# Kernel optimization log

Measured on AMD Instinct MI355X. Metric: run time of the kernel, lower is better.

## Reference

```python
import jax, jax.numpy as jnp
import numpy as np

HEADS = 16
D_K = 64  # hidden_units // heads


def setup_inputs() -> dict:
    key = jax.random.key(0)
    ks = jax.random.split(key, 9)
    B, S, D, H = 4, 2048, 1024, 1024  # batch, seq, in_shape, hidden_units
    inputs = jax.random.normal(ks[0], (B, S, D), dtype=jnp.float32)
    # xavier_normal for weights, default bias init ~ small uniform (use zeros for simplicity of baseline? keep uniform like torch)
    def xavier(k, fan_in, fan_out):
        std = jnp.sqrt(2.0 / (fan_in + fan_out))
        return jax.random.normal(k, (fan_out, fan_in), dtype=jnp.float32) * std
    Wq = xavier(ks[1], D, H)
    Wk = xavier(ks[2], D, H)
    Wv = xavier(ks[3], D, H)
    Wo = xavier(ks[4], H, H)
    bound = 1.0 / jnp.sqrt(D)
    bq = jax.random.uniform(ks[5], (H,), minval=-bound, maxval=bound, dtype=jnp.float32)
    bk = jax.random.uniform(ks[6], (H,), minval=-bound, maxval=bound, dtype=jnp.float32)
    bv = jax.random.uniform(ks[7], (H,), minval=-bound, maxval=bound, dtype=jnp.float32)
    bo = jax.random.uniform(ks[8], (H,), minval=-1.0 / jnp.sqrt(H), maxval=1.0 / jnp.sqrt(H), dtype=jnp.float32)
    return {"inputs": inputs, "Wq": Wq, "bq": bq, "Wk": Wk, "bk": bk,
            "Wv": Wv, "bv": bv, "Wo": Wo, "bo": bo}


def reference(inputs, Wq, bq, Wk, bk, Wv, bv, Wo, bo):
    B, S, _ = inputs.shape
    # QKV projections -> (B, S, heads, d_k)
    def proj(W, b):
        return (inputs @ W.T + b).reshape(B, S, HEADS, D_K)
    q = proj(Wq, bq)
    k = proj(Wk, bk)
    v = proj(Wv, bv)
    scale = 1.0 / jnp.sqrt(jnp.float32(D_K))
    # scores: (B, heads, S, S)
    scores = jnp.einsum('bqhd,bkhd->bhqk', q, k) * scale
    attn = jax.nn.softmax(scores, axis=-1)
    # (B, heads, S, d_k) -> (B, S, heads*d_k)
    ctx = jnp.einsum('bhqk,bkhd->bqhd', attn, v).reshape(B, S, HEADS * D_K)
    out = ctx @ Wo.T + bo
    return out
```

## Files before the change

kernel.cpp:

```cpp
#include <hip/hip_runtime.h>
#include <stdint.h>


using bf16x8 = __attribute__((ext_vector_type(8))) short;
using f32x4  = __attribute__((ext_vector_type(4))) float;
using u32x4  = __attribute__((ext_vector_type(4))) unsigned;

#define QSCALE 0.18033688f

__device__ __forceinline__ unsigned short f2bf(float f) {
    unsigned u = __builtin_bit_cast(unsigned, f);
    u += 0x7fffu + ((u >> 16) & 1u);
    return (unsigned short)(u >> 16);
}

__device__ __forceinline__ unsigned pack2bf(float f0, float f1) {
    unsigned u0 = __builtin_bit_cast(unsigned, f0) + 0x8000u;
    unsigned u1 = __builtin_bit_cast(unsigned, f1) + 0x8000u;
    return __builtin_amdgcn_perm(u1, u0, 0x07060302);
}

__device__ __forceinline__ void gld16(const void* g, void* l) {
    void* gnc = (void*)g;
    __builtin_amdgcn_global_load_lds((__attribute__((address_space(1))) void*)gnc,
                                     (__attribute__((address_space(3))) void*)l,
                                     16, 0, 0);
}

__device__ __forceinline__ int swz(int R, int g) {
    return R * 64 + ((g ^ (R & 7)) << 3);
}

__global__ void castall(const float* __restrict__ X, const float* __restrict__ Wq,
                        const float* __restrict__ Wk, const float* __restrict__ Wv,
                        const float* __restrict__ Wo, unsigned short* __restrict__ Xb,
                        unsigned short* __restrict__ Wqkvb, unsigned short* __restrict__ Wob) {
    const int bx = blockIdx.x;
    const float* src; unsigned short* dst; int idx;
    if (bx < 8192) { src = X; dst = Xb; idx = bx * 256 + threadIdx.x; }
    else {
        const int r = bx - 8192, w = r >> 10;
        idx = (r & 1023) * 256 + threadIdx.x;
        src = (w == 0) ? Wq : (w == 1) ? Wk : (w == 2) ? Wv : Wo;
        dst = (w == 3) ? Wob : Wqkvb + (size_t)w * 1048576;
    }
    float4 v = ((const float4*)src)[idx];
    ((uint2*)dst)[idx] = make_uint2(pack2bf(v.x, v.y), pack2bf(v.z, v.w));
}

__global__ __launch_bounds__(512, 2) void gemm_qkv(const unsigned short* __restrict__ A,
                                                   const unsigned short* __restrict__ Wqkv,
                                                   const float* __restrict__ bq,
                                                   const float* __restrict__ bk,
                                                   const float* __restrict__ bv,
                                                   unsigned short* __restrict__ Qb,
                                                   unsigned short* __restrict__ Kb,
                                                   unsigned short* __restrict__ Vt) {
    __shared__ alignas(16) unsigned short smem[65536];

    const int tid  = threadIdx.x;
    const int lane = tid & 63;
    const int w    = tid >> 6;
    const int quad = lane >> 4;
    const int l15  = lane & 15;
    const int lr   = lane >> 3;
    const int lcs  = (((lane & 7) ^ lr) << 3);
    const int wm   = w >> 2;
    const int wn   = w & 3;

    int wg = blockIdx.x;
    wg = (wg & 7) * 48 + (wg >> 3);
    const int bxx = wg % 12, byy = wg / 12;
    const int col0 = bxx * 256;
    const int row0 = byy * 256;

    const unsigned short* aS = A    + (size_t)(row0 + w * 16 + lr) * 1024 + lcs;
    const unsigned short* bS = Wqkv + (size_t)(col0 + w * 16 + lr) * 1024 + lcs;
    const int dstW = w * 1024;

#define STG_A(t_, h_, b_)                                                              \
    { const unsigned short* s_ = aS + (size_t)(h_) * 131072 + (t_) * 64;               \
      gld16(s_,            &smem[(b_) * 32768 + (h_) * 8192 + dstW]);                  \
      gld16(s_ + 8 * 1024, &smem[(b_) * 32768 + (h_) * 8192 + dstW + 512]); }
#define STG_B(t_, h_, b_)                                                              \
    { const unsigned short* s_ = bS + (size_t)(h_) * 131072 + (t_) * 64;               \
      gld16(s_,            &smem[(b_) * 32768 + 16384 + (h_) * 8192 + dstW]);          \
      gld16(s_ + 8 * 1024, &smem[(b_) * 32768 + 16384 + (h_) * 8192 + dstW + 512]); }

    f32x4 acc[8][4];
#pragma unroll
    for (int i = 0; i < 8; i++)
#pragma unroll
        for (int j = 0; j < 4; j++) acc[i][j] = f32x4{0.f, 0.f, 0.f, 0.f};

    STG_A(0, 0, 0) STG_A(0, 1, 0) STG_B(0, 0, 0) STG_B(0, 1, 0)
    STG_B(1, 0, 1) STG_B(1, 1, 1)
    asm volatile("s_waitcnt vmcnt(4)" ::: "memory");
    __builtin_amdgcn_s_barrier();

    for (int t = 0; t < 16; ++t) {
        const int b = t & 1;
        unsigned short* bufA = smem + b * 32768;
        unsigned short* bufB = bufA + 16384;
        bf16x8 bfr[4][2];
#pragma unroll
        for (int p = 0; p < 4; ++p) {
            bf16x8 afr[2][2];
            if (p == 0) {
#pragma unroll
                for (int nf = 0; nf < 4; ++nf)
#pragma unroll
                    for (int kx = 0; kx < 2; ++kx)
                        bfr[nf][kx] = *(const bf16x8*)&bufB[swz(wn * 64 + nf * 16 + l15, kx * 4 + quad)];
            }
#pragma unroll
            for (int mi = 0; mi < 2; ++mi)
#pragma unroll
                for (int kx = 0; kx < 2; ++kx)
                    afr[mi][kx] = *(const bf16x8*)&bufA[swz(wm * 128 + (p * 2 + mi) * 16 + l15, kx * 4 + quad)];

            if (p == 0)      { if (t < 15) STG_A(t + 1, 0, b ^ 1) }
            else if (p == 1) { if (t < 15) STG_A(t + 1, 1, b ^ 1) }
            else if (p == 2) { if (t < 14) STG_B(t + 2, 0, b) }
            else {
                if (t < 14) {
                    STG_B(t + 2, 1, b)
                    asm volatile("s_waitcnt vmcnt(4)" ::: "memory");
                } else if (t == 14) {
                    asm volatile("s_waitcnt vmcnt(0)" ::: "memory");
                }
            }
            __builtin_amdgcn_s_barrier();
            __builtin_amdgcn_s_setprio(1);
#pragma unroll
            for (int kx = 0; kx < 2; ++kx)
#pragma unroll
                for (int mi = 0; mi < 2; ++mi)
#pragma unroll
                    for (int nf = 0; nf < 4; ++nf)
                        acc[p * 2 + mi][nf] = __builtin_amdgcn_mfma_f32_16x16x32_bf16(
                            afr[mi][kx], bfr[nf][kx], acc[p * 2 + mi][nf], 0, 0, 0);
            __builtin_amdgcn_s_setprio(0);
            __builtin_amdgcn_s_barrier();
        }
    }
#undef STG_A
#undef STG_B

    const int nb   = col0 >> 10;
    const int colq = col0 & 1023;
    const float* bias = (nb == 0) ? bq : (nb == 1) ? bk : bv;

    if (nb != 2) {
        const float sc = (nb == 0) ? QSCALE : 1.0f;
        unsigned short* C = (nb == 0) ? Qb : Kb;
#pragma unroll
        for (int h = 0; h < 2; ++h) {
            if (wm == h) {
#pragma unroll
                for (int mf = 0; mf < 8; ++mf)
#pragma unroll
                    for (int nf = 0; nf < 4; ++nf) {
                        const int ct  = wn * 64 + nf * 16 + l15;
                        const float bvv = bias[colq + ct];
                        const int rt  = mf * 16 + quad * 4;
#pragma unroll
                        for (int r = 0; r < 4; ++r)
                            smem[(rt + r) * 264 + ct] = f2bf((acc[mf][nf][r] + bvv) * sc);
                    }
            }
            __syncthreads();
            const int rr = tid >> 2, qq = tid & 3;
            unsigned short* gdst = C + (size_t)(row0 + h * 128 + rr) * 1024 + colq + qq * 64;
#pragma unroll
            for (int j = 0; j < 8; ++j)
                *(bf16x8*)(gdst + j * 8) = *(const bf16x8*)&smem[rr * 264 + qq * 64 + j * 8];
            if (h == 0) __syncthreads();
        }
    } else {
        const int bb = row0 >> 11, s0 = row0 & 2047;
#pragma unroll
        for (int h = 0; h < 2; ++h) {
            if (wm == h) {
#pragma unroll
                for (int mf = 0; mf < 8; ++mf)
#pragma unroll
                    for (int nf = 0; nf < 4; ++nf) {
                        const int ct  = wn * 64 + nf * 16 + l15;
                        const float bvv = bias[colq + ct];
                        const int st  = mf * 16 + quad * 4;
                        *(uint2*)&smem[ct * 136 + st] =
                            make_uint2(pack2bf(acc[mf][nf][0] + bvv, acc[mf][nf][1] + bvv),
                                       pack2bf(acc[mf][nf][2] + bvv, acc[mf][nf][3] + bvv));
                    }
            }
            __syncthreads();
            const int c = tid >> 1, hs = tid & 1;
            unsigned short* gdst = Vt + ((size_t)(bb * 1024 + colq + c)) * 2048 + s0 + h * 128 + hs * 64;
#pragma unroll
            for (int j = 0; j < 8; ++j)
                *(bf16x8*)(gdst + j * 8) = *(const bf16x8*)&smem[c * 136 + hs * 64 + j * 8];
            if (h == 0) __syncthreads();
        }
    }
}

__global__ __launch_bounds__(256) void gemm_out(const unsigned short* __restrict__ A,
                                                const unsigned short* __restrict__ W,
                                                const float* __restrict__ bias,
                                                float* __restrict__ C) {
    __shared__ alignas(16) unsigned short sA[128 * 64];
    __shared__ alignas(16) unsigned short sB[128 * 64];
    const int tid  = threadIdx.x;
    const int lane = tid & 63;
    const int wave = tid >> 6;
    const int quad = lane >> 4;
    const int l15  = lane & 15;
    const int lr   = lane >> 3;
    const int lcs  = (((lane & 7) ^ lr) << 3);
    const int row0 = blockIdx.y * 128;
    const int col0 = blockIdx.x * 128;
    const int wm = wave >> 1, wn = wave & 1;

    f32x4 acc[4][4];
#pragma unroll
    for (int i = 0; i < 4; i++)
#pragma unroll
        for (int j = 0; j < 4; j++) acc[i][j] = f32x4{0.f, 0.f, 0.f, 0.f};

    for (int kt = 0; kt < 16; ++kt) {
        const int k0 = kt * 64;
#pragma unroll
        for (int i = 0; i < 4; i++) {
            const int c = wave * 4 + i;
            const int r = c * 8 + lr;
            gld16(A + (size_t)(row0 + r) * 1024 + k0 + lcs, &sA[c * 512]);
            gld16(W + (size_t)(col0 + r) * 1024 + k0 + lcs, &sB[c * 512]);
        }
        __syncthreads();
#pragma unroll
        for (int kx = 0; kx < 2; ++kx) {
            bf16x8 a[4], b[4];
#pragma unroll
            for (int i = 0; i < 4; i++) {
                a[i] = *(const bf16x8*)&sA[swz(wm * 64 + i * 16 + l15, kx * 4 + quad)];
                b[i] = *(const bf16x8*)&sB[swz(wn * 64 + i * 16 + l15, kx * 4 + quad)];
            }
#pragma unroll
            for (int i = 0; i < 4; i++)
#pragma unroll
                for (int j = 0; j < 4; j++)
                    acc[i][j] = __builtin_amdgcn_mfma_f32_16x16x32_bf16(a[i], b[j], acc[i][j], 0, 0, 0);
        }
        __syncthreads();
    }

#pragma unroll
    for (int i = 0; i < 4; i++) {
#pragma unroll
        for (int j = 0; j < 4; j++) {
            const int col   = col0 + wn * 64 + j * 16 + l15;
            const float bvv = bias[col];
            const int rbase = row0 + wm * 64 + i * 16 + quad * 4;
#pragma unroll
            for (int r = 0; r < 4; r++)
                C[(size_t)(rbase + r) * 1024 + col] = acc[i][j][r] + bvv;
        }
    }
}

__global__ __launch_bounds__(512, 4) void attn(const unsigned short* __restrict__ Q,
                                               const unsigned short* __restrict__ K,
                                               const unsigned short* __restrict__ Vt,
                                               unsigned short* __restrict__ Ctx) {
    __shared__ alignas(16) unsigned short Kl[2][4096];
    __shared__ alignas(16) unsigned short Vl[2][4096];

    const int tid  = threadIdx.x;
    const int lane = tid & 63;
    const int wave = tid >> 6;
    const int quad = lane >> 4;
    const int l15  = lane & 15;
    const int lr   = lane >> 3;
    const int lcs  = (((lane & 7) ^ lr) << 3);

    const int qt = blockIdx.x, h = blockIdx.y, b = blockIdx.z;
    const int q0 = qt * 256;
    const size_t tokbase = (size_t)b * 2048;

    bf16x8 qa[2][2];
#pragma unroll
    for (int mt = 0; mt < 2; ++mt)
#pragma unroll
        for (int kx = 0; kx < 2; ++kx)
            qa[mt][kx] = *(const bf16x8*)(Q + (tokbase + q0 + wave * 32 + mt * 16 + l15) * 1024 +
                                          h * 64 + kx * 32 + quad * 8);

    f32x4 O[2][4], Osum[2];
#pragma unroll
    for (int mt = 0; mt < 2; ++mt) {
#pragma unroll
        for (int nt = 0; nt < 4; ++nt) O[mt][nt] = f32x4{0.f, 0.f, 0.f, 0.f};
        Osum[mt] = f32x4{0.f, 0.f, 0.f, 0.f};
    }
    const bf16x8 vones = {16256, 16256, 16256, 16256, 16256, 16256, 16256, 16256};

#define AT_STAGE(kt_, buf_)                                                                     \
    {                                                                                           \
        const int rr = wave * 8 + lr;                                                           \
        gld16(K + (tokbase + (kt_) * 64 + rr) * 1024 + h * 64 + lcs, &Kl[buf_][wave * 512]);    \
        gld16(Vt + ((size_t)(b * 1024 + h * 64 + rr)) * 2048 + (kt_) * 64 + lcs,                \
              &Vl[buf_][wave * 512]);                                                           \
    }

    AT_STAGE(0, 0)
    for (int kt = 0; kt < 32; ++kt) {
        const int buf = kt & 1;
        __syncthreads();
        if (kt < 31) AT_STAGE(kt + 1, buf ^ 1)

        f32x4 St[4][2];
#pragma unroll
        for (int nt = 0; nt < 4; ++nt)
#pragma unroll
            for (int mt = 0; mt < 2; ++mt) St[nt][mt] = f32x4{0.f, 0.f, 0.f, 0.f};
#pragma unroll
        for (int kx = 0; kx < 2; ++kx) {
            bf16x8 kb[4];
#pragma unroll
            for (int nt = 0; nt < 4; ++nt)
                kb[nt] = *(const bf16x8*)&Kl[buf][swz(nt * 16 + l15, kx * 4 + quad)];
#pragma unroll
            for (int nt = 0; nt < 4; ++nt)
#pragma unroll
                for (int mt = 0; mt < 2; ++mt)
                    St[nt][mt] = __builtin_amdgcn_mfma_f32_16x16x32_bf16(kb[nt], qa[mt][kx], St[nt][mt], 0, 0, 0);
        }

        unsigned d0[4][2], d1[4][2];
#pragma unroll
        for (int mt = 0; mt < 2; ++mt) {
#pragma unroll
            for (int nt = 0; nt < 4; ++nt) {
                float p0 = __builtin_amdgcn_exp2f(St[nt][mt][0]);
                float p1 = __builtin_amdgcn_exp2f(St[nt][mt][1]);
                float p2 = __builtin_amdgcn_exp2f(St[nt][mt][2]);
                float p3 = __builtin_amdgcn_exp2f(St[nt][mt][3]);
                d0[nt][mt] = pack2bf(p0, p1);
                d1[nt][mt] = pack2bf(p2, p3);
            }
        }

        bf16x8 pa[2][2];
#pragma unroll
        for (int mt = 0; mt < 2; ++mt) {
#pragma unroll
            for (int kx = 0; kx < 2; ++kx) {
                auto rA = __builtin_amdgcn_permlane32_swap(d0[2 * kx][mt], d0[2 * kx + 1][mt], false, false);
                auto sA = __builtin_amdgcn_permlane16_swap(rA[0], rA[1], false, false);
                auto rB = __builtin_amdgcn_permlane32_swap(d1[2 * kx][mt], d1[2 * kx + 1][mt], false, false);
                auto sB = __builtin_amdgcn_permlane16_swap(rB[0], rB[1], false, false);
                u32x4 t = {sA[0], sB[0], sA[1], sB[1]};
                pa[mt][kx] = __builtin_bit_cast(bf16x8, t);
            }
        }

#pragma unroll
        for (int kx = 0; kx < 2; ++kx) {
            bf16x8 vb[4];
#pragma unroll
            for (int nt = 0; nt < 4; ++nt)
                vb[nt] = *(const bf16x8*)&Vl[buf][swz(nt * 16 + l15, kx * 4 + quad)];
#pragma unroll
            for (int mt = 0; mt < 2; ++mt) {
#pragma unroll
                for (int nt = 0; nt < 4; ++nt)
                    O[mt][nt] = __builtin_amdgcn_mfma_f32_16x16x32_bf16(pa[mt][kx], vb[nt], O[mt][nt], 0, 0, 0);
                Osum[mt] = __builtin_amdgcn_mfma_f32_16x16x32_bf16(pa[mt][kx], vones, Osum[mt], 0, 0, 0);
            }
        }
    }
#undef AT_STAGE

#pragma unroll
    for (int mt = 0; mt < 2; ++mt) {
#pragma unroll
        for (int r = 0; r < 4; ++r) {
            const float inv = 1.0f / Osum[mt][r];
            const int row   = q0 + wave * 32 + mt * 16 + quad * 4 + r;
            const size_t base = (tokbase + row) * 1024 + h * 64;
#pragma unroll
            for (int nt = 0; nt < 4; ++nt)
                Ctx[base + nt * 16 + l15] = f2bf(O[mt][nt][r] * inv);
        }
    }
}

extern "C" void kernel_launch(void* const* d_in, const int* in_sizes, int n_in,
                              void* d_out, int out_size, void* d_ws, size_t ws_size,
                              hipStream_t stream) {
    (void)in_sizes; (void)n_in; (void)out_size; (void)ws_size;
    const float* X  = (const float*)d_in[0];
    const float* Wq = (const float*)d_in[1];
    const float* bq = (const float*)d_in[2];
    const float* Wk = (const float*)d_in[3];
    const float* bk = (const float*)d_in[4];
    const float* Wv = (const float*)d_in[5];
    const float* bv = (const float*)d_in[6];
    const float* Wo = (const float*)d_in[7];
    const float* bo = (const float*)d_in[8];

    char* ws = (char*)d_ws;
    unsigned short* Xb    = (unsigned short*)(ws);
    unsigned short* Qb    = (unsigned short*)(ws + (size_t)16 * 1048576);
    unsigned short* Kb    = (unsigned short*)(ws + (size_t)32 * 1048576);
    unsigned short* Vt    = (unsigned short*)(ws + (size_t)48 * 1048576);
    unsigned short* Wqkvb = (unsigned short*)(ws + (size_t)64 * 1048576);
    unsigned short* Wob   = (unsigned short*)(ws + (size_t)70 * 1048576);
    unsigned short* Ctx   = Xb;

    castall<<<dim3(12288), 256, 0, stream>>>(X, Wq, Wk, Wv, Wo, Xb, Wqkvb, Wob);
    gemm_qkv<<<dim3(384), 512, 0, stream>>>(Xb, Wqkvb, bq, bk, bv, Qb, Kb, Vt);
    attn<<<dim3(8, 16, 4), 512, 0, stream>>>(Qb, Kb, Vt, Ctx);
    gemm_out<<<dim3(8, 64), 256, 0, stream>>>(Ctx, Wob, bo, (float*)d_out);
}
```

Baseline: 279.1 us.

## Rewrite output GEMM with 128x256 tiles, double-buffered async loads and remapped blocks

The output projection GEMM moves from 128x128 tiles with 256 threads and a load-then-sync loop to 128x256 tiles with 512 threads. It double-buffers LDS with prefetch one or two k-steps ahead, uses explicit vmcnt waits and barriers, raises wave priority around the MFMA sections, and remaps block indices for cache locality. The attention kernel also precomputes its swizzled LDS offsets and starts the first score MFMA from zero instead of zero-initialising the accumulators. The aim is to hide global-load latency and cut sync stalls in gemm_out, at the cost of a 96KB LDS footprint and more complex manual synchronisation.

After: 274.8 us. Within noise of the previous version (-1.5%).

```diff
diff --git a/kernel.cpp b/kernel.cpp
--- a/kernel.cpp
+++ b/kernel.cpp
@@ -205,12 +205,113 @@
     }
 }
 
-__global__ __launch_bounds__(256) void gemm_out(const unsigned short* __restrict__ A,
-                                                const unsigned short* __restrict__ W,
-                                                const float* __restrict__ bias,
-                                                float* __restrict__ C) {
-    __shared__ alignas(16) unsigned short sA[128 * 64];
-    __shared__ alignas(16) unsigned short sB[128 * 64];
+__global__ __launch_bounds__(512, 2) void gemm_out(const unsigned short* __restrict__ A,
+                                                   const unsigned short* __restrict__ W,
+                                                   const float* __restrict__ bias,
+                                                   float* __restrict__ C) {
+    __shared__ alignas(16) unsigned short smem[49152];
+
+    const int tid  = threadIdx.x;
+    const int lane = tid & 63;
+    const int w    = tid >> 6;
+    const int quad = lane >> 4;
+    const int l15  = lane & 15;
+    const int lr   = lane >> 3;
+    const int lcs  = (((lane & 7) ^ lr) << 3);
+    const int wm   = w >> 2;
+    const int wn   = w & 3;
+
+    int wg = blockIdx.x;
+    wg = (wg & 7) * 32 + (wg >> 3);
+    const int col0 = (wg & 3) * 256;
+    const int row0 = (wg >> 2) * 128;
+
+    const unsigned short* aS = A + (size_t)(row0 + w * 16 + lr) * 1024 + lcs;
+    const unsigned short* bS = W + (size_t)(col0 + w * 16 + lr) * 1024 + lcs;
+    const int dstW = w * 1024;
+
+#define STG_AO(t_, b_)                                                                  \
+    { const unsigned short* s_ = aS + (t_) * 64;                                        \
+      gld16(s_,            &smem[(b_) * 24576 + dstW]);                                 \
+      gld16(s_ + 8 * 1024, &smem[(b_) * 24576 + dstW + 512]); }
+#define STG_BO(t_, h_, b_)                                                              \
+    { const unsigned short* s_ = bS + (size_t)(h_) * 131072 + (t_) * 64;                \
+      gld16(s_,            &smem[(b_) * 24576 + 8192 + (h_) * 8192 + dstW]);            \
+      gld16(s_ + 8 * 1024, &smem[(b_) * 24576 + 8192 + (h_) * 8192 + dstW + 512]); }
+
+    f32x4 acc[4][4];
+#pragma unroll
+    for (int i = 0; i < 4; i++)
+#pragma unroll
+        for (int j = 0; j < 4; j++) acc[i][j] = f32x4{0.f, 0.f, 0.f, 0.f};
+
+    STG_AO(0, 0) STG_BO(0, 0, 0) STG_BO(0, 1, 0)
+    STG_BO(1, 0, 1) STG_BO(1, 1, 1)
+    asm volatile("s_waitcnt vmcnt(4)" ::: "memory");
+    __builtin_amdgcn_s_barrier();
+
+    for (int t = 0; t < 16; ++t) {
+        const int b = t & 1;
+        unsigned short* bufA = smem + b * 24576;
+        unsigned short* bufB = bufA + 8192;
+        bf16x8 bfr[4][2];
+#pragma unroll
+        for (int p = 0; p < 4; ++p) {
+            bf16x8 afr[2];
+            if (p == 0) {
+#pragma unroll
+                for (int nf = 0; nf < 4; ++nf)
+#pragma unroll
+                    for (int kx = 0; kx < 2; ++kx)
+                        bfr[nf][kx] = *(const bf16x8*)&bufB[swz(wn * 64 + nf * 16 + l15, kx * 4 + quad)];
+            }
+#pragma unroll
+            for (int kx = 0; kx < 2; ++kx)
+                afr[kx] = *(const bf16x8*)&bufA[swz(wm * 64 + p * 16 + l15, kx * 4 + quad)];
+
+            if (p == 0)      { if (t < 15) STG_AO(t + 1, b ^ 1) }
+            else if (p == 1) { if (t < 14) STG_BO(t + 2, 0, b) }
+            else if (p == 2) { if (t < 14) STG_BO(t + 2, 1, b) }
+            else {
+                if (t < 14)      { asm volatile("s_waitcnt vmcnt(4)" ::: "memory"); }
+                else if (t == 14){ asm volatile("s_waitcnt vmcnt(0)" ::: "memory"); }
+            }
+            __builtin_amdgcn_s_barrier();
+            __builtin_amdgcn_s_setprio(1);
+#pragma unroll
+            for (int kx = 0; kx < 2; ++kx)
+#pragma unroll
+                for (int nf = 0; nf < 4; ++nf)
+                    acc[p][nf] = __builtin_amdgcn_mfma_f32_16x16x32_bf16(
+                        afr[kx], bfr[nf][kx], acc[p][nf], 0, 0, 0);
+            __builtin_amdgcn_s_setprio(0);
+            __builtin_amdgcn_s_barrier();
+        }
+    }
+#undef STG_AO
+#undef STG_BO
+
+#pragma unroll
+    for (int mf = 0; mf < 4; ++mf) {
+#pragma unroll
+        for (int nf = 0; nf < 4; ++nf) {
+            const int col   = col0 + wn * 64 + nf * 16 + l15;
+            const float bvv = bias[col];
+            const int rbase = row0 + wm * 64 + mf * 16 + quad * 4;
+#pragma unroll
+            for (int r = 0; r < 4; r++)
+                C[(size_t)(rbase + r) * 1024 + col] = acc[mf][nf][r] + bvv;
+        }
+    }
+}
+
+__global__ __launch_bounds__(512, 4) void attn(const unsigned short* __restrict__ Q,
+                                               const unsigned short* __restrict__ K,
+                                               const unsigned short* __restrict__ Vt,
+                                               unsigned short* __restrict__ Ctx) {
+    __shared__ alignas(16) unsigned short Kl[2][4096];
+    __shared__ alignas(16) unsigned short Vl[2][4096];
+
     const int tid  = threadIdx.x;
     const int lane = tid & 63;
     const int wave = tid >> 6;
@@ -218,76 +319,14 @@
     const int l15  = lane & 15;
     const int lr   = lane >> 3;
     const int lcs  = (((lane & 7) ^ lr) << 3);
-    const int row0 = blockIdx.y * 128;
-    const int col0 = blockIdx.x * 128;
-    const int wm = wave >> 1, wn = wave & 1;
-
-    f32x4 acc[4][4];
-#pragma unroll
-    for (int i = 0; i < 4; i++)
-#pragma unroll
-        for (int j = 0; j < 4; j++) acc[i][j] = f32x4{0.f, 0.f, 0.f, 0.f};
-
-    for (int kt = 0; kt < 16; ++kt) {
-        const int k0 = kt * 64;
-#pragma unroll
-        for (int i = 0; i < 4; i++) {
-            const int c = wave * 4 + i;
-            const int r = c * 8 + lr;
-            gld16(A + (size_t)(row0 + r) * 1024 + k0 + lcs, &sA[c * 512]);
-            gld16(W + (size_t)(col0 + r) * 1024 + k0 + lcs, &sB[c * 512]);
-        }
-        __syncthreads();
-#pragma unroll
-        for (int kx = 0; kx < 2; ++kx) {
-            bf16x8 a[4], b[4];
-#pragma unroll
-            for (int i = 0; i < 4; i++) {
-                a[i] = *(const bf16x8*)&sA[swz(wm * 64 + i * 16 + l15, kx * 4 + quad)];
-                b[i] = *(const bf16x8*)&sB[swz(wn * 64 + i * 16 + l15, kx * 4 + quad)];
-            }
-#pragma unroll
-            for (int i = 0; i < 4; i++)
-#pragma unroll
-                for (int j = 0; j < 4; j++)
-                    acc[i][j] = __builtin_amdgcn_mfma_f32_16x16x32_bf16(a[i], b[j], acc[i][j], 0, 0, 0);
-        }
-        __syncthreads();
-    }
-
-#pragma unroll
-    for (int i = 0; i < 4; i++) {
-#pragma unroll
-        for (int j = 0; j < 4; j++) {
-            const int col   = col0 + wn * 64 + j * 16 + l15;
-            const float bvv = bias[col];
-            const int rbase = row0 + wm * 64 + i * 16 + quad * 4;
-#pragma unroll
-            for (int r = 0; r < 4; r++)
-                C[(size_t)(rbase + r) * 1024 + col] = acc[i][j][r] + bvv;
-        }
-    }
-}
-
-__global__ __launch_bounds__(512, 4) void attn(const unsigned short* __restrict__ Q,
-                                               const unsigned short* __restrict__ K,
-                                               const unsigned short* __restrict__ Vt,
-                                               unsigned short* __restrict__ Ctx) {
-    __shared__ alignas(16) unsigned short Kl[2][4096];
-    __shared__ alignas(16) unsigned short Vl[2][4096];
-
-    const int tid  = threadIdx.x;
-    const int lane = tid & 63;
-    const int wave = tid >> 6;
-    const int quad = lane >> 4;
-    const int l15  = lane & 15;
-    const int lr   = lane >> 3;
-    const int lcs  = (((lane & 7) ^ lr) << 3);
 
     const int qt = blockIdx.x, h = blockIdx.y, b = blockIdx.z;
     const int q0 = qt * 256;
     const size_t tokbase = (size_t)b * 2048;
 
+    const int lo0 = l15 * 64 + (((quad    ) ^ (l15 & 7)) << 3);
+    const int lo1 = l15 * 64 + (((quad + 4) ^ (l15 & 7)) << 3);
+
     bf16x8 qa[2][2];
 #pragma unroll
     for (int mt = 0; mt < 2; ++mt)
@@ -303,6 +342,7 @@
         for (int nt = 0; nt < 4; ++nt) O[mt][nt] = f32x4{0.f, 0.f, 0.f, 0.f};
         Osum[mt] = f32x4{0.f, 0.f, 0.f, 0.f};
     }
+    const f32x4 z4 = {0.f, 0.f, 0.f, 0.f};
     const bf16x8 vones = {16256, 16256, 16256, 16256, 16256, 16256, 16256, 16256};
 
 #define AT_STAGE(kt_, buf_)                                                                     \
@@ -318,23 +358,28 @@
         const int buf = kt & 1;
         __syncthreads();
         if (kt < 31) AT_STAGE(kt + 1, buf ^ 1)
+        const unsigned short* kb_base = &Kl[buf][0];
+        const unsigned short* vb_base = &Vl[buf][0];
 
         f32x4 St[4][2];
-#pragma unroll
-        for (int nt = 0; nt < 4; ++nt)
-#pragma unroll
-            for (int mt = 0; mt < 2; ++mt) St[nt][mt] = f32x4{0.f, 0.f, 0.f, 0.f};
-#pragma unroll
-        for (int kx = 0; kx < 2; ++kx) {
+        {
             bf16x8 kb[4];
 #pragma unroll
             for (int nt = 0; nt < 4; ++nt)
-                kb[nt] = *(const bf16x8*)&Kl[buf][swz(nt * 16 + l15, kx * 4 + quad)];
+                kb[nt] = *(const bf16x8*)&kb_base[lo0 + nt * 1024];
 #pragma unroll
             for (int nt = 0; nt < 4; ++nt)
 #pragma unroll
                 for (int mt = 0; mt < 2; ++mt)
-                    St[nt][mt] = __builtin_amdgcn_mfma_f32_16x16x32_bf16(kb[nt], qa[mt][kx], St[nt][mt], 0, 0, 0);
+                    St[nt][mt] = __builtin_amdgcn_mfma_f32_16x16x32_bf16(kb[nt], qa[mt][0], z4, 0, 0, 0);
+#pragma unroll
+            for (int nt = 0; nt < 4; ++nt)
+                kb[nt] = *(const bf16x8*)&kb_base[lo1 + nt * 1024];
+#pragma unroll
+            for (int nt = 0; nt < 4; ++nt)
+#pragma unroll
+                for (int mt = 0; mt < 2; ++mt)
+                    St[nt][mt] = __builtin_amdgcn_mfma_f32_16x16x32_bf16(kb[nt], qa[mt][1], St[nt][mt], 0, 0, 0);
         }
 
         unsigned d0[4][2], d1[4][2];
@@ -370,7 +415,7 @@
             bf16x8 vb[4];
 #pragma unroll
             for (int nt = 0; nt < 4; ++nt)
-                vb[nt] = *(const bf16x8*)&Vl[buf][swz(nt * 16 + l15, kx * 4 + quad)];
+                vb[nt] = *(const bf16x8*)&vb_base[(kx ? lo1 : lo0) + nt * 1024];
 #pragma unroll
             for (int mt = 0; mt < 2; ++mt) {
 #pragma unroll
@@ -422,5 +467,5 @@
     castall<<<dim3(12288), 256, 0, stream>>>(X, Wq, Wk, Wv, Wo, Xb, Wqkvb, Wob);
     gemm_qkv<<<dim3(384), 512, 0, stream>>>(Xb, Wqkvb, bq, bk, bv, Qb, Kb, Vt);
     attn<<<dim3(8, 16, 4), 512, 0, stream>>>(Qb, Kb, Vt, Ctx);
-    gemm_out<<<dim3(8, 64), 256, 0, stream>>>(Ctx, Wob, bo, (float*)d_out);
-}
+    gemm_out<<<dim3(256), 512, 0, stream>>>(Ctx, Wob, bo, (float*)d_out);
+}
```
